# Kernel optimization log

Measured on AMD Instinct MI355X. Metric: run time of the kernel, lower is better.

The kernel has to match this reference:

```python
import jax, jax.numpy as jnp
import numpy as np

B, C, T = 64, 64, 4096
SFREQ = 256.0
NYQ = SFREQ / 2.0
NF = 2            # n_filters = len(filter_f_mean)
NOUT = 4
F_BINS = T // 2 + 1
N_FEAT = NF * C * (C - 1) // 2


def setup_inputs() -> dict:
    key = jax.random.key(0)
    kx, kw = jax.random.split(key)
    x = jax.random.normal(kx, (B, C, T), dtype=jnp.float32)
    # learned filter params (normalized exactly as in __init__)
    f_mean = jnp.full((NF,), 23.0 / NYQ, dtype=jnp.float32)
    bandwidth = jnp.full((NF,), 44.0 / NYQ, dtype=jnp.float32)
    shape_p = jnp.full((NF,), 2.0, dtype=jnp.float32)
    group_delay = jnp.full((NF,), 20.0 / 1000.0, dtype=jnp.float32)
    lin_w = jax.random.normal(kw, (NOUT, N_FEAT), dtype=jnp.float32) / np.sqrt(N_FEAT)
    lin_b = jnp.zeros((NOUT,), dtype=jnp.float32)
    return dict(x=x, f_mean=f_mean, bandwidth=bandwidth, shape_p=shape_p,
                group_delay=group_delay, lin_w=lin_w, lin_b=lin_b)


def _construct_filters(f_mean, bandwidth, shape_p, group_delay):
    # normalized frequency grid: fftfreq[:T//2] ++ [nyquist], / nyquist
    freqs = np.fft.fftfreq(T, d=1.0 / SFREQ)[: T // 2]
    n_range = jnp.asarray(np.concatenate([freqs, [NYQ]]) / NYQ, dtype=jnp.float32)  # (F,)
    fm = jnp.clip(f_mean, 1.0 / NYQ, 45.0 / NYQ)[:, None]        # (NF,1)
    bw = jnp.clip(bandwidth, 1.0 / NYQ, 1.0)[:, None]
    p = (jnp.clip(shape_p, 2.0, 3.0) * 8.0 - 14.0)[:, None]      # shape*8-14
    log2 = jnp.log(jnp.float32(2.0))
    scale = bw / (2.0 * log2 ** (1.0 / p))
    mag = jnp.exp(-(((jnp.abs(n_range[None, :] - fm)) + 1e-8) / scale) ** p)  # (NF,F)
    mag = mag / jnp.max(mag, axis=-1, keepdims=True)
    phase = jnp.linspace(0.0, SFREQ, F_BINS, dtype=jnp.float32)
    pha = -group_delay[:, None] * phase[None, :] * jnp.pi
    return mag * jnp.cos(pha), mag * jnp.sin(pha)  # (NF,F) each


def _eegminer_plv(x, f_mean, bandwidth, shape_p, group_delay, lin_w, lin_b):
    filt_re, filt_im = _construct_filters(f_mean, bandwidth, shape_p, group_delay)
    X = jnp.fft.rfft(x, axis=-1)  # (B,C,F) complex
    # NOTE: torch multiplies the view_as_real tensor by the (real, imag) filter
    # stack COMPONENT-WISE (not a complex multiply); reproduce that faithfully.
    re = X.real[:, :, None, :] * filt_re[None, None]  # (B,C,NF,F)
    im = X.imag[:, :, None, :] * filt_im[None, None]
    re = jnp.transpose(re, (0, 2, 1, 3))  # (B,NF,C,F)
    im = jnp.transpose(im, (0, 2, 1, 3))
    # hilbert_freq(forward_fourier=False): double all bins, halve DC, zero-pad to T
    dc_scale = jnp.where(jnp.arange(F_BINS) == 0, 1.0, 2.0).astype(x.dtype)
    pad = ((0, 0), (0, 0), (0, 0), (0, T - F_BINS))  # T - F = F - 2
    z = jnp.pad(re * dc_scale, pad) + 1j * jnp.pad(im * dc_scale, pad)
    analytic = jnp.fft.ifft(z, axis=-1)  # (B,NF,C,T) complex
    amp = jnp.sqrt(analytic.real ** 2 + analytic.imag ** 2 + 1e-6)
    ur = analytic.real / amp
    ui = analytic.imag / amp
    rr = jnp.einsum('bfct,bfdt->bfcd', ur, ur)
    ii = jnp.einsum('bfct,bfdt->bfcd', ui, ui)
    ri = jnp.einsum('bfct,bfdt->bfcd', ur, ui)
    ir = jnp.einsum('bfct,bfdt->bfcd', ui, ur)
    corr_re = rr + ii
    corr_im = ri - ir
    plv = jnp.sqrt(corr_re ** 2 + corr_im ** 2 + 1e-6) / T  # (B,NF,C,C)
    plv = jnp.transpose(plv, (0, 2, 3, 1))  # (B,C,C,NF)
    iu, ju = np.triu_indices(C, 1)
    feats = plv[:, iu, ju, :].reshape(x.shape[0], N_FEAT)
    # BatchNorm1d(affine=False), training mode: batch stats, biased var, eps=1e-5
    mu = jnp.mean(feats, axis=0)
    var = jnp.mean((feats - mu) ** 2, axis=0)
    feats = (feats - mu) / jnp.sqrt(var + 1e-5)
    return feats @ lin_w.T + lin_b


def reference(x, f_mean, bandwidth, shape_p, group_delay, lin_w, lin_b):
    return _eegminer_plv(x, f_mean, bandwidth, shape_p, group_delay, lin_w, lin_b)
```

## Files before the change

kernel.cpp:

```cpp
#include <hip/hip_runtime.h>
#include <math.h>

#define T_N     4096
#define B_N     64
#define C_N     64
#define NFILT   2
#define F_BINS  2049
#define NPAIRS  2016
#define NFEAT   4032
#define NOUT    4
#define TSG     4
#define NKS     32
#define XSLOTS  2304

#define PI_F 3.14159265358979323846f

typedef _Float16 f16x8 __attribute__((ext_vector_type(8)));
typedef _Float16 f16x2 __attribute__((ext_vector_type(2)));
typedef float    f32x4 __attribute__((ext_vector_type(4)));
typedef float    cplx  __attribute__((ext_vector_type(2)));


#define OFF_U     65536
#define G_BYTES   (128 * TSG * 12288 * 4)

__global__ __launch_bounds__(256) void filter_kernel(
    const float* __restrict__ fm_, const float* __restrict__ bw_,
    const float* __restrict__ sp_, const float* __restrict__ gd_,
    float* __restrict__ filt) {
  __shared__ float smag[F_BINS];
  __shared__ float sred[256];
  const int tid = threadIdx.x;
  for (int f = 0; f < NFILT; ++f) {
    float* Fre = filt + f * 8192;
    float* Fim = Fre + 4096;
    for (int p = tid; p < 4096; p += 256) { Fre[p] = 0.0f; Fim[p] = 0.0f; }
    const float fm = fminf(fmaxf(fm_[f], 1.0f / 128.0f), 45.0f / 128.0f);
    const float bw = fminf(fmaxf(bw_[f], 1.0f / 128.0f), 1.0f);
    const float pp = fminf(fmaxf(sp_[f], 2.0f), 3.0f) * 8.0f - 14.0f;
    const float gd = gd_[f];
    const float scale = bw / (2.0f * powf(0.69314718055994531f, 1.0f / pp));
    float lmax = 0.0f;
    for (int i = tid; i < F_BINS; i += 256) {
      const float n = (float)i / 2048.0f;
      const float m = expf(-powf((fabsf(n - fm) + 1e-8f) / scale, pp));
      smag[i] = m;
      lmax = fmaxf(lmax, m);
    }
    sred[tid] = lmax;
    __syncthreads();
    for (int s = 128; s > 0; s >>= 1) {
      if (tid < s) sred[tid] = fmaxf(sred[tid], sred[tid + s]);
      __syncthreads();
    }
    const float inv = 1.0f / sred[0];
    __syncthreads();
    for (int k = tid; k < F_BINS; k += 256) {
      const float m = smag[k] * inv;
      const float pha = -gd * ((float)k * 0.125f) * PI_F;
      float sn, cs;
      sincosf(pha, &sn, &cs);
      const float dcs = (k == 0) ? 1.0f : 2.0f;
      const float sT = dcs * (1.0f / (float)T_N);
      const int p = (k & 0xF00) + ((k & 15) << 4) + ((k >> 4) & 15);
      Fre[p] = m * cs * sT;
      Fim[p] = m * sn * sT;
    }
    __syncthreads();
  }
}

__device__ __forceinline__ cplx cmul(cplx a, cplx w) {
  return cplx{a.x, a.x} * w + cplx{-a.y, a.y} * cplx{w.y, w.x};
}
__device__ __forceinline__ cplx twid(float rev) {
  return cplx{__builtin_amdgcn_cosf(rev), __builtin_amdgcn_sinf(rev)};
}

template<int SGN>
__device__ __forceinline__ void dft16(cplx* __restrict__ v) {
  const float sg = (float)SGN;
  const float C1 = 0.923879532511287f, S1 = 0.382683432365090f;
  const float Hh = 0.707106781186548f;
  cplx g[16];
#pragma unroll
  for (int n2 = 0; n2 < 4; ++n2) {
    const cplx a = v[n2], b = v[4 + n2], c = v[8 + n2], d = v[12 + n2];
    const cplx t0 = a + c, t1 = a - c, t2 = b + d, t3 = b - d;
    const cplx it3 = (SGN < 0) ? cplx{t3.y, -t3.x} : cplx{-t3.y, t3.x};
    g[n2]      = t0 + t2;
    g[8 + n2]  = t0 - t2;
    g[4 + n2]  = t1 + it3;
    g[12 + n2] = t1 - it3;
  }
  g[5]  = cmul(g[5],  cplx{C1,  sg * S1});
  g[6]  = cmul(g[6],  cplx{Hh,  sg * Hh});
  g[7]  = cmul(g[7],  cplx{S1,  sg * C1});
  g[9]  = cmul(g[9],  cplx{Hh,  sg * Hh});
  g[10] = (SGN < 0) ? cplx{g[10].y, -g[10].x} : cplx{-g[10].y, g[10].x};
  g[11] = cmul(g[11], cplx{-Hh, sg * Hh});
  g[13] = cmul(g[13], cplx{S1,  sg * C1});
  g[14] = cmul(g[14], cplx{-Hh, sg * Hh});
  g[15] = cmul(g[15], cplx{-C1, -sg * S1});
#pragma unroll
  for (int k1 = 0; k1 < 4; ++k1) {
    const cplx a = g[4 * k1], b = g[4 * k1 + 1];
    const cplx c = g[4 * k1 + 2], d = g[4 * k1 + 3];
    const cplx t0 = a + c, t1 = a - c, t2 = b + d, t3 = b - d;
    const cplx it3 = (SGN < 0) ? cplx{t3.y, -t3.x} : cplx{-t3.y, t3.x};
    v[k1]      = t0 + t2;
    v[8 + k1]  = t0 - t2;
    v[4 + k1]  = t1 + it3;
    v[12 + k1] = t1 - it3;
  }
}

__device__ __forceinline__ void tr_cross_fwd(cplx* __restrict__ v,
                                             cplx* __restrict__ lds, int t) {
  __syncthreads();
#pragma unroll
  for (int k = 0; k < 16; ++k) lds[k * 264 + t] = v[k];
  __syncthreads();
  const int base = (t >> 4) * 264 + (t & 15);
#pragma unroll
  for (int m = 0; m < 16; ++m) v[m] = lds[base + m * 16];
}
__device__ __forceinline__ void tr_cross_inv(cplx* __restrict__ v,
                                             cplx* __restrict__ lds, int t) {
  __syncthreads();
  const int base = (t >> 4) * 264 + (t & 15);
#pragma unroll
  for (int m = 0; m < 16; ++m) lds[base + m * 16] = v[m];
  __syncthreads();
#pragma unroll
  for (int k = 0; k < 16; ++k) v[k] = lds[k * 264 + t];
}
__device__ __forceinline__ void tr_group(cplx* __restrict__ v,
                                         cplx* __restrict__ lds, int t) {
  __syncthreads();
  const int k1 = t >> 4, s = t & 15;
  const int rowb = k1 * 264;
#pragma unroll
  for (int r = 0; r < 16; ++r)
    lds[rowb + r * 16 + ((s + r) & 15)] = v[r];
  __syncthreads();
#pragma unroll
  for (int a = 0; a < 16; ++a)
    v[a] = lds[rowb + s * 16 + ((a + s) & 15)];
}

__global__ __launch_bounds__(256) void fwd_kernel(
    const float* __restrict__ x, f16x2* __restrict__ Xs, int chunkbase) {
  const int cp = blockIdx.x & 31;
  const int bb = blockIdx.x >> 5;
  const int b  = chunkbase + bb;
  const int t  = threadIdx.x;
  const int j1 = t & 15;
  __shared__ cplx lds[16 * 264];
  __shared__ cplx TB[256];

  TB[t] = twid(-(float)((t >> 4) * (t & 15)) * (1.0f / 256.0f));

  cplx v[16];
  const float* xp0 = x + ((size_t)(b * C_N + 2 * cp)) * T_N;
  const float* xp1 = xp0 + T_N;
#pragma unroll
  for (int r = 0; r < 16; ++r)
    v[r] = cplx{xp0[r * 256 + t], xp1[r * 256 + t]};

  dft16<-1>(v);
#pragma unroll
  for (int k = 1; k < 16; ++k) {
    v[k] = cmul(v[k], twid((float)(t * k) * (-1.0f / 4096.0f)));
  }
  tr_cross_fwd(v, lds, t);
  dft16<-1>(v);
#pragma unroll
  for (int k = 1; k < 16; ++k)
    v[k] = cmul(v[k], TB[k * 16 + j1]);
  tr_group(v, lds, t);
  dft16<-1>(v);

  __syncthreads();
#pragma unroll
  for (int q = 0; q < 16; ++q) lds[q * 264 + t] = v[q];
  __syncthreads();
  const int k1 = t >> 4;
  const int tp = (k1 == 0) ? ((16 - j1) & 15)
                           : (((16 - k1) << 4) | (15 - j1));
  f16x2* Xp0 = Xs + (size_t)(bb * C_N + 2 * cp) * XSLOTS;
  f16x2* Xp1 = Xp0 + XSLOTS;
#pragma unroll
  for (int q = 0; q < 9; ++q) {
    const int qp = (t == 0) ? ((16 - q) & 15) : (15 - q);
    const cplx Z  = v[q];
    const cplx Zp = lds[qp * 264 + tp];
    f16x2 h0, h1;
    h0[0] = (_Float16)(0.5f * (Z.x + Zp.x));
    h0[1] = (_Float16)(0.5f * (Z.y - Zp.y));
    h1[0] = (_Float16)(0.5f * (Z.y + Zp.y));
    h1[1] = (_Float16)(0.5f * (Zp.x - Z.x));
    Xp0[q * 256 + t] = h0;
    Xp1[q * 256 + t] = h1;
  }
}

__global__ __launch_bounds__(256) void inv_kernel(
    const f16x2* __restrict__ Xs, const float* __restrict__ filt,
    _Float16* __restrict__ Urg, _Float16* __restrict__ Uig) {
  const int f  = blockIdx.x & 1;
  const int c  = (blockIdx.x >> 1) & 63;
  const int bb = blockIdx.x >> 7;
  const int t  = threadIdx.x;
  const int j1 = t & 15;
  __shared__ cplx lds[16 * 264];
  __shared__ cplx TB[256];
  __shared__ cplx TCB[256];
  __shared__ cplx TCS[16];

  {
    const int prod = (t >> 4) * (t & 15);
    TB[t]  = twid((float)prod * (1.0f / 256.0f));
    TCB[t] = twid((float)prod * (1.0f / 4096.0f));
    if (t < 16) TCS[t] = twid((float)t * (1.0f / 256.0f));
  }

  cplx v[16];
  const f16x2* Xp = Xs + (size_t)(bb * C_N + c) * XSLOTS;
  const float* Fre = filt + f * 8192;
  const float* Fim = Fre + 4096;
#pragma unroll
  for (int q = 0; q < 9; ++q) {
    const f16x2 xv = Xp[q * 256 + t];
    v[q] = cplx{(float)xv[0] * Fre[q * 256 + t],
                (float)xv[1] * Fim[q * 256 + t]};
  }
#pragma unroll
  for (int q = 9; q < 16; ++q)
    v[q] = cplx{0.0f, 0.0f};

  __syncthreads();

  dft16<1>(v);
#pragma unroll
  for (int k = 1; k < 16; ++k)
    v[k] = cmul(v[k], TB[k * 16 + j1]);
  tr_group(v, lds, t);
  dft16<1>(v);
  {
    cplx w = TCB[t];
    v[0] = cmul(v[0], w);
    const cplx st = TCS[t >> 4];
#pragma unroll
    for (int m1 = 1; m1 < 16; ++m1) {
      w = cmul(w, st);
      v[m1] = cmul(v[m1], w);
    }
  }
  tr_cross_inv(v, lds, t);
  dft16<1>(v);

  const int sl = bb * 2 + f;
  _Float16* upr = Urg + ((size_t)sl * C_N + c) * T_N;
  _Float16* upi = Uig + ((size_t)sl * C_N + c) * T_N;
#pragma unroll
  for (int n1 = 0; n1 < 16; ++n1) {
    const float ir = rsqrtf(v[n1].x * v[n1].x + v[n1].y * v[n1].y + 1e-6f);
    upr[n1 * 256 + t] = (_Float16)(v[n1].x * ir);
    upi[n1 * 256 + t] = (_Float16)(v[n1].y * ir);
  }
}

__global__ __launch_bounds__(256) void gram_kernel(
    const _Float16* __restrict__ Urg, const _Float16* __restrict__ Uig,
    float* __restrict__ Gp, int slicebase) {
  const int sl = blockIdx.x / TSG;
  const int ts = blockIdx.x % TSG;
  const int tid = threadIdx.x;
  const int w = tid >> 6;
  const int lane = tid & 63;
  __shared__ _Float16 sUr[2][64 * 40], sUi[2][64 * 40];

  const int row = tid >> 2, quarter = tid & 3;
  const size_t goff = (size_t)sl * C_N * T_N + (size_t)row * T_N
                      + ts * (T_N / TSG) + quarter * 8;
  const int loff = row * 40 + quarter * 8;
  const int frow = (lane & 15) * 40 + (lane >> 4) * 8;
  const int aoff = w * 640 + frow;

  f32x4 accRr[4] = {}, accIi[4] = {}, accRi[4] = {};

  f16x8 rr = *(const f16x8*)&Urg[goff];
  f16x8 ri = *(const f16x8*)&Uig[goff];
  int cur = 0;
  for (int ks = 0; ks < NKS; ++ks) {
    *(f16x8*)&sUr[cur][loff] = rr;
    *(f16x8*)&sUi[cur][loff] = ri;
    if (ks + 1 < NKS) {
      rr = *(const f16x8*)&Urg[goff + (ks + 1) * 32];
      ri = *(const f16x8*)&Uig[goff + (ks + 1) * 32];
    }
    __syncthreads();
    const f16x8 ar = *(const f16x8*)&sUr[cur][aoff];
    const f16x8 ai = *(const f16x8*)&sUi[cur][aoff];
#pragma unroll
    for (int n = 0; n < 4; ++n) {
      const f16x8 br = *(const f16x8*)&sUr[cur][n * 640 + frow];
      const f16x8 bi = *(const f16x8*)&sUi[cur][n * 640 + frow];
      accRr[n] = __builtin_amdgcn_mfma_f32_16x16x32_f16(ar, br, accRr[n], 0, 0, 0);
      accIi[n] = __builtin_amdgcn_mfma_f32_16x16x32_f16(ai, bi, accIi[n], 0, 0, 0);
      accRi[n] = __builtin_amdgcn_mfma_f32_16x16x32_f16(ar, bi, accRi[n], 0, 0, 0);
    }
    cur ^= 1;
  }

  float* Gs = Gp + (size_t)((slicebase + sl) * TSG + ts) * 12288;
  const int r0 = w * 16 + (lane >> 4) * 4;
  const int c0 = lane & 15;
#pragma unroll
  for (int n = 0; n < 4; ++n) {
    const bool upper = (n >= w);
#pragma unroll
    for (int e = 0; e < 4; ++e) {
      const int idx = (r0 + e) * 64 + n * 16 + c0;
      if (upper) {
        Gs[idx] = accRr[n][e];
        Gs[4096 + idx] = accIi[n][e];
      }
      Gs[8192 + idx] = accRi[n][e];
    }
  }
}

__global__ __launch_bounds__(256) void plv_kernel(
    const float* __restrict__ Gp, float* __restrict__ feats) {
  const int idx = blockIdx.x * 256 + threadIdx.x;
  if (idx >= B_N * NFILT * NPAIRS) return;
  const int slice = idx / NPAIRS;
  const int p = idx - slice * NPAIRS;
  const int b = slice >> 1, f = slice & 1;
  int c = 0, rem = p;
  while (rem >= 63 - c) { rem -= 63 - c; ++c; }
  const int d = c + 1 + rem;
  const float* Gs = Gp + (size_t)slice * TSG * 12288;
  float rr = 0, ii = 0, ri = 0, ir = 0;
#pragma unroll
  for (int ts = 0; ts < TSG; ++ts) {
    const float* P = Gs + ts * 12288;
    rr += P[c * 64 + d];
    ii += P[4096 + c * 64 + d];
    ri += P[8192 + c * 64 + d];
    ir += P[8192 + d * 64 + c];
  }
  const float cre = rr + ii;
  const float cim = ri - ir;
  const float plv = sqrtf(cre * cre + cim * cim + 1e-6f) * (1.0f / (float)T_N);
  feats[b * NFEAT + p * NFILT + f] = plv;
}

__global__ __launch_bounds__(256) void stats_kernel(
    const float* __restrict__ feats, float* __restrict__ stats) {
  const int j = blockIdx.x * 256 + threadIdx.x;
  if (j >= NFEAT) return;
  float s = 0.0f;
  for (int b = 0; b < B_N; ++b) s += feats[b * NFEAT + j];
  const float mu = s * (1.0f / (float)B_N);
  float v = 0.0f;
  for (int b = 0; b < B_N; ++b) {
    const float d = feats[b * NFEAT + j] - mu;
    v += d * d;
  }
  v *= (1.0f / (float)B_N);
  stats[j] = mu;
  stats[NFEAT + j] = 1.0f / sqrtf(v + 1e-5f);
}

__global__ __launch_bounds__(256) void out_kernel(
    const float* __restrict__ feats, const float* __restrict__ stats,
    const float* __restrict__ w, const float* __restrict__ lb,
    float* __restrict__ out) {
  const int b = blockIdx.x;
  const int tid = threadIdx.x;
  float acc0 = 0, acc1 = 0, acc2 = 0, acc3 = 0;
  for (int j = tid; j < NFEAT; j += 256) {
    const float v = (feats[b * NFEAT + j] - stats[j]) * stats[NFEAT + j];
    acc0 += v * w[0 * NFEAT + j];
    acc1 += v * w[1 * NFEAT + j];
    acc2 += v * w[2 * NFEAT + j];
    acc3 += v * w[3 * NFEAT + j];
  }
  __shared__ float red[4][256];
  red[0][tid] = acc0; red[1][tid] = acc1; red[2][tid] = acc2; red[3][tid] = acc3;
  __syncthreads();
  for (int s = 128; s > 0; s >>= 1) {
    if (tid < s) {
#pragma unroll
      for (int o = 0; o < 4; ++o) red[o][tid] += red[o][tid + s];
    }
    __syncthreads();
  }
  if (tid < 4) out[b * NOUT + tid] = red[tid][0] + lb[tid];
}

extern "C" void kernel_launch(void* const* d_in, const int* in_sizes, int n_in,
                              void* d_out, int out_size, void* d_ws, size_t ws_size,
                              hipStream_t stream) {
  const float* x  = (const float*)d_in[0];
  const float* fm = (const float*)d_in[1];
  const float* bw = (const float*)d_in[2];
  const float* sp = (const float*)d_in[3];
  const float* gd = (const float*)d_in[4];
  const float* lw = (const float*)d_in[5];
  const float* lb = (const float*)d_in[6];
  float* out = (float*)d_out;
  char* base = (char*)d_ws;

  const size_t perCB = 2 * 1048576 + (size_t)C_N * XSLOTS * 4;
  const size_t fixed = OFF_U + (size_t)G_BYTES + (size_t)B_N * NFEAT * 4 + 2 * NFEAT * 4;
  int CB = 64;
  if (ws_size < fixed + (size_t)64 * perCB) CB = 32;
  if (ws_size < fixed + (size_t)32 * perCB) CB = 16;
  const int nchunk = B_N / CB;

  const size_t u_bytes = (size_t)CB * 1048576;
  const size_t x_bytes = (size_t)CB * C_N * XSLOTS * 4;
  float*    filt  = (float*)base;
  _Float16* Urg   = (_Float16*)(base + OFF_U);
  _Float16* Uig   = (_Float16*)(base + OFF_U + u_bytes);
  f16x2*    Xs    = (f16x2*)(base + OFF_U + 2 * u_bytes);
  float*    Gp    = (float*)(base + OFF_U + 2 * u_bytes + x_bytes);
  float*    feats = (float*)(base + OFF_U + 2 * u_bytes + x_bytes + G_BYTES);
  float*    stats = feats + (size_t)B_N * NFEAT;

  filter_kernel<<<1, 256, 0, stream>>>(fm, bw, sp, gd, filt);

  for (int chunk = 0; chunk < nchunk; ++chunk) {
    fwd_kernel<<<CB * (C_N / 2), 256, 0, stream>>>(x, Xs, chunk * CB);
    inv_kernel<<<CB * C_N * NFILT, 256, 0, stream>>>(Xs, filt, Urg, Uig);
    gram_kernel<<<CB * 2 * TSG, 256, 0, stream>>>(Urg, Uig, Gp, chunk * CB * 2);
  }

  plv_kernel<<<(B_N * NFILT * NPAIRS + 255) / 256, 256, 0, stream>>>(Gp, feats);
  stats_kernel<<<(NFEAT + 255) / 256, 256, 0, stream>>>(feats, stats);
  out_kernel<<<B_N, 256, 0, stream>>>(feats, stats, lw, lb, out);
}
```

Before: 143.7 us.

## Parallelize filter build, table-drive twiddles, closed-form pair index, reshape cmul

Four small changes ship together. The filter kernel now runs one block per filter instead of looping over both filters in a single block. The inverse FFT's chained twiddle recurrence is replaced by independent products against a 256-entry table, which breaks a serial dependency but adds LDS reads. The pair index in plv_kernel comes from a sqrt-based closed form instead of a linear while loop, and cmul is rewritten with explicit shuffles that may compile to packed FMA.

```diff
diff --git a/kernel.cpp b/kernel.cpp
--- a/kernel.cpp
+++ b/kernel.cpp
@@ -31,47 +31,47 @@
   __shared__ float smag[F_BINS];
   __shared__ float sred[256];
   const int tid = threadIdx.x;
-  for (int f = 0; f < NFILT; ++f) {
-    float* Fre = filt + f * 8192;
-    float* Fim = Fre + 4096;
-    for (int p = tid; p < 4096; p += 256) { Fre[p] = 0.0f; Fim[p] = 0.0f; }
-    const float fm = fminf(fmaxf(fm_[f], 1.0f / 128.0f), 45.0f / 128.0f);
-    const float bw = fminf(fmaxf(bw_[f], 1.0f / 128.0f), 1.0f);
-    const float pp = fminf(fmaxf(sp_[f], 2.0f), 3.0f) * 8.0f - 14.0f;
-    const float gd = gd_[f];
-    const float scale = bw / (2.0f * powf(0.69314718055994531f, 1.0f / pp));
-    float lmax = 0.0f;
-    for (int i = tid; i < F_BINS; i += 256) {
-      const float n = (float)i / 2048.0f;
-      const float m = expf(-powf((fabsf(n - fm) + 1e-8f) / scale, pp));
-      smag[i] = m;
-      lmax = fmaxf(lmax, m);
-    }
-    sred[tid] = lmax;
+  const int f = blockIdx.x;
+  float* Fre = filt + f * 8192;
+  float* Fim = Fre + 4096;
+  for (int p = tid; p < 4096; p += 256) { Fre[p] = 0.0f; Fim[p] = 0.0f; }
+  const float fm = fminf(fmaxf(fm_[f], 1.0f / 128.0f), 45.0f / 128.0f);
+  const float bw = fminf(fmaxf(bw_[f], 1.0f / 128.0f), 1.0f);
+  const float pp = fminf(fmaxf(sp_[f], 2.0f), 3.0f) * 8.0f - 14.0f;
+  const float gd = gd_[f];
+  const float scale = bw / (2.0f * powf(0.69314718055994531f, 1.0f / pp));
+  float lmax = 0.0f;
+  for (int i = tid; i < F_BINS; i += 256) {
+    const float n = (float)i / 2048.0f;
+    const float m = expf(-powf((fabsf(n - fm) + 1e-8f) / scale, pp));
+    smag[i] = m;
+    lmax = fmaxf(lmax, m);
+  }
+  sred[tid] = lmax;
+  __syncthreads();
+  for (int s = 128; s > 0; s >>= 1) {
+    if (tid < s) sred[tid] = fmaxf(sred[tid], sred[tid + s]);
     __syncthreads();
-    for (int s = 128; s > 0; s >>= 1) {
-      if (tid < s) sred[tid] = fmaxf(sred[tid], sred[tid + s]);
-      __syncthreads();
-    }
-    const float inv = 1.0f / sred[0];
-    __syncthreads();
-    for (int k = tid; k < F_BINS; k += 256) {
-      const float m = smag[k] * inv;
-      const float pha = -gd * ((float)k * 0.125f) * PI_F;
-      float sn, cs;
-      sincosf(pha, &sn, &cs);
-      const float dcs = (k == 0) ? 1.0f : 2.0f;
-      const float sT = dcs * (1.0f / (float)T_N);
-      const int p = (k & 0xF00) + ((k & 15) << 4) + ((k >> 4) & 15);
-      Fre[p] = m * cs * sT;
-      Fim[p] = m * sn * sT;
-    }
-    __syncthreads();
+  }
+  const float inv = 1.0f / sred[0];
+  for (int k = tid; k < F_BINS; k += 256) {
+    const float m = smag[k] * inv;
+    const float pha = -gd * ((float)k * 0.125f) * PI_F;
+    float sn, cs;
+    sincosf(pha, &sn, &cs);
+    const float dcs = (k == 0) ? 1.0f : 2.0f;
+    const float sT = dcs * (1.0f / (float)T_N);
+    const int p = (k & 0xF00) + ((k & 15) << 4) + ((k >> 4) & 15);
+    Fre[p] = m * cs * sT;
+    Fim[p] = m * sn * sT;
   }
 }
 
 __device__ __forceinline__ cplx cmul(cplx a, cplx w) {
-  return cplx{a.x, a.x} * w + cplx{-a.y, a.y} * cplx{w.y, w.x};
+  const cplx wx = __builtin_shufflevector(w, w, 0, 0);
+  const cplx wy = __builtin_shufflevector(w, w, 1, 1);
+  const cplx as = __builtin_shufflevector(a, a, 1, 0);
+  return cplx{-as.x, as.y} * wy + a * wx;
 }
 __device__ __forceinline__ cplx twid(float rev) {
   return cplx{__builtin_amdgcn_cosf(rev), __builtin_amdgcn_sinf(rev)};
@@ -216,13 +216,13 @@
   __shared__ cplx lds[16 * 264];
   __shared__ cplx TB[256];
   __shared__ cplx TCB[256];
-  __shared__ cplx TCS[16];
+  __shared__ cplx TCS2[256];
 
   {
     const int prod = (t >> 4) * (t & 15);
-    TB[t]  = twid((float)prod * (1.0f / 256.0f));
-    TCB[t] = twid((float)prod * (1.0f / 4096.0f));
-    if (t < 16) TCS[t] = twid((float)t * (1.0f / 256.0f));
+    TB[t]   = twid((float)prod * (1.0f / 256.0f));
+    TCB[t]  = twid((float)prod * (1.0f / 4096.0f));
+    TCS2[t] = twid((float)((t >> 4) * (t & 15)) * (1.0f / 256.0f));
   }
 
   cplx v[16];
@@ -248,12 +248,12 @@
   tr_group(v, lds, t);
   dft16<1>(v);
   {
-    cplx w = TCB[t];
-    v[0] = cmul(v[0], w);
-    const cplx st = TCS[t >> 4];
+    const cplx tcb = TCB[t];
+    const int k1 = t >> 4;
+    v[0] = cmul(v[0], tcb);
 #pragma unroll
     for (int m1 = 1; m1 < 16; ++m1) {
-      w = cmul(w, st);
+      const cplx w = cmul(tcb, TCS2[m1 * 16 + k1]);
       v[m1] = cmul(v[m1], w);
     }
   }
@@ -339,9 +339,12 @@
   const int slice = idx / NPAIRS;
   const int p = idx - slice * NPAIRS;
   const int b = slice >> 1, f = slice & 1;
-  int c = 0, rem = p;
-  while (rem >= 63 - c) { rem -= 63 - c; ++c; }
-  const int d = c + 1 + rem;
+  const int r = NPAIRS - 1 - p;
+  int m = (int)((sqrtf((float)(8 * r + 1)) - 1.0f) * 0.5f);
+  while ((m + 1) * (m + 2) / 2 <= r) ++m;
+  while (m * (m + 1) / 2 > r) --m;
+  const int c = 62 - m;
+  const int d = 63 - (r - m * (m + 1) / 2);
   const float* Gs = Gp + (size_t)slice * TSG * 12288;
   float rr = 0, ii = 0, ri = 0, ir = 0;
 #pragma unroll
@@ -432,7 +435,7 @@
   float*    feats = (float*)(base + OFF_U + 2 * u_bytes + x_bytes + G_BYTES);
   float*    stats = feats + (size_t)B_N * NFEAT;
 
-  filter_kernel<<<1, 256, 0, stream>>>(fm, bw, sp, gd, filt);
+  filter_kernel<<<NFILT, 256, 0, stream>>>(fm, bw, sp, gd, filt);
 
   for (int chunk = 0; chunk < nchunk; ++chunk) {
     fwd_kernel<<<CB * (C_N / 2), 256, 0, stream>>>(x, Xs, chunk * CB);
```

Result: faster. 137.1 us (-4.6%).
